# Optimization experiments

Hardware: AMD Instinct MI355X
Metric: run time of the kernel (lower is better)

The kernel has to match this reference:

```python
import jax, jax.numpy as jnp
import numpy as np

HEADS = 16
HEAD_DIM = 64
EMBED = HEADS * HEAD_DIM  # 1024
B, S = 2, 2048


def setup_inputs() -> dict:
    key = jax.random.key(0)
    ks = jax.random.split(key, 9)
    return {
        "value": jax.random.normal(ks[0], (B, S, EMBED), dtype=jnp.float32),
        "key": jax.random.normal(ks[1], (B, S, EMBED), dtype=jnp.float32),
        "query": jax.random.normal(ks[2], (B, S, EMBED), dtype=jnp.float32),
        "mask": jax.random.randint(ks[3], (B, 1, S, S), 0, 2, dtype=jnp.int32),
        "Wq": jax.random.normal(ks[4], (HEAD_DIM, HEAD_DIM), dtype=jnp.float32) * 0.02,
        "Wk": jax.random.normal(ks[5], (HEAD_DIM, HEAD_DIM), dtype=jnp.float32) * 0.02,
        "Wv": jax.random.normal(ks[6], (HEAD_DIM, HEAD_DIM), dtype=jnp.float32) * 0.02,
        "Wo": jax.random.normal(ks[7], (EMBED, EMBED), dtype=jnp.float32) * 0.02,
        "bo": jnp.zeros((EMBED,), dtype=jnp.float32),
    }


def reference(value, key, query, mask, Wq, Wk, Wv, Wo, bo):
    N, Lv = value.shape[0], value.shape[1]
    Lk, Lq = key.shape[1], query.shape[1]
    # Faithful to original: plain reshape (N, heads, len, head_dim), NOT transpose.
    v = value.reshape(N, HEADS, Lv, HEAD_DIM)
    k = key.reshape(N, HEADS, Lk, HEAD_DIM)
    q = query.reshape(N, HEADS, Lq, HEAD_DIM)
    # Per-head Linear (no bias): x @ W.T
    V = jnp.einsum('bhld,ed->bhle', v, Wv)
    K = jnp.einsum('bhld,ed->bhle', k, Wk)
    Q = jnp.einsum('bhld,ed->bhle', q, Wq)
    score = jnp.einsum('bhqd,bhkd->bhqk', Q, K)  # [B,H,Sq,Sk]
    score = jnp.where(mask == 0, jnp.float32(-1e20), score)
    # Faithful quirk: scale by sqrt(embed_size), not sqrt(head_dim)
    scale = jnp.float32(EMBED ** 0.5)
    attn = jax.nn.softmax(score / scale, axis=3)
    out = jnp.einsum('bhqk,bhkd->bhqd', attn, V).reshape(N, Lq, HEADS * HEAD_DIM)
    return out @ Wo.T + bo
```

## Files before the change

kernel.cpp:

```cpp
#include <hip/hip_runtime.h>
#include <hip/hip_bf16.h>
#include <cstdint>
#include <cstddef>

#define S_LEN 2048
#define N_HEADS 16
#define HD 64
#define EMB 1024
#define N_BATCH 2
#define N_BH (N_BATCH * N_HEADS)

typedef __attribute__((ext_vector_type(4))) float f32x4;
typedef __attribute__((ext_vector_type(8))) short short8;
typedef __attribute__((ext_vector_type(8))) _Float16 half8;
typedef __attribute__((ext_vector_type(2))) _Float16 half2v;

__device__ __forceinline__ f32x4 mfma16h(half8 a, half8 b, f32x4 c) {
    return __builtin_amdgcn_mfma_f32_16x16x32_f16(a, b, c, 0, 0, 0);
}

__device__ __forceinline__ unsigned pkh(float a, float b) {
    return __builtin_bit_cast(unsigned, __builtin_amdgcn_cvt_pkrtz(a, b));
}

#if __has_builtin(__builtin_amdgcn_exp2f)
__device__ __forceinline__ float fast_exp2(float x) { return __builtin_amdgcn_exp2f(x); }
#else
__device__ __forceinline__ float fast_exp2(float x) { return exp2f(x); }
#endif

__global__ __launch_bounds__(256) void prep_kernel(
    const float* __restrict__ q_in, const float* __restrict__ k_in,
    const float* __restrict__ v_in,
    const float* __restrict__ Wq, const float* __restrict__ Wk,
    const float* __restrict__ Wv, const float* __restrict__ Wo,
    const int* __restrict__ mask,
    short* __restrict__ Qb, short* __restrict__ Kb, short* __restrict__ Vt,
    short* __restrict__ Woh, unsigned long long* __restrict__ bits) {
    __shared__ short Al[64 * 72];
    __shared__ short Wl[64 * 72];
    __shared__ short Ol[64 * 72];
    int bx = blockIdx.x;
    int t = threadIdx.x;

    if (bx >= 3072) {
        if (bx < 11264) {
            int wid = ((bx - 3072) * 256 + t) >> 6;
            int lane = t & 63;
            const int* src = mask + (size_t)wid * 256 + lane;
            unsigned long long w0 = __ballot(src[0] != 0);
            unsigned long long w1 = __ballot(src[64] != 0);
            unsigned long long w2 = __ballot(src[128] != 0);
            unsigned long long w3 = __ballot(src[192] != 0);
            if (lane == 0) {
                unsigned long long* dst = bits + (size_t)wid * 4;
                dst[0] = w0; dst[1] = w1; dst[2] = w2; dst[3] = w3;
            }
        } else {
            int i = (bx - 11264) * 256 + t;
            f32x4 a = reinterpret_cast<const f32x4*>(Wo)[i * 2];
            f32x4 b = reinterpret_cast<const f32x4*>(Wo)[i * 2 + 1];
            uint4 u = { pkh(a.x, a.y), pkh(a.z, a.w), pkh(b.x, b.y), pkh(b.z, b.w) };
            reinterpret_cast<uint4*>(Woh)[i] = u;
        }
        return;
    }

    int rt = bx & 31;
    int bh = (bx >> 5) & 31;
    int tz = bx >> 10;
    const float* src = (tz == 0 ? q_in : tz == 1 ? k_in : v_in)
                       + (size_t)bh * S_LEN * HD + (size_t)rt * 64 * HD;
    const float* W = (tz == 0 ? Wq : tz == 1 ? Wk : Wv);

#pragma unroll
    for (int r = 0; r < 4; r++) {
        int f4 = t + 256 * r;
        int row = f4 >> 4;
        int c4 = (f4 & 15) * 4;
        f32x4 a = reinterpret_cast<const f32x4*>(src)[f4];
        uint2 ua = { pkh(a.x, a.y), pkh(a.z, a.w) };
        *reinterpret_cast<uint2*>(&Al[row * 72 + c4]) = ua;
        f32x4 w = reinterpret_cast<const f32x4*>(W)[f4];
        uint2 uw = { pkh(w.x, w.y), pkh(w.z, w.w) };
        *reinterpret_cast<uint2*>(&Wl[row * 72 + c4]) = uw;
    }
    __syncthreads();

    int wave = t >> 6, lane = t & 63, quad = lane >> 4, col = lane & 15;
    half8 a0 = *reinterpret_cast<const half8*>(&Al[(wave * 16 + col) * 72 + quad * 8]);
    half8 a1 = *reinterpret_cast<const half8*>(&Al[(wave * 16 + col) * 72 + 32 + quad * 8]);

    const float C1 = 0.04508422002777448f;
    float scl = (tz == 0) ? C1 : 1.0f;

    f32x4 acc[4];
#pragma unroll
    for (int jt = 0; jt < 4; jt++) {
        half8 b0 = *reinterpret_cast<const half8*>(&Wl[(jt * 16 + col) * 72 + quad * 8]);
        half8 b1 = *reinterpret_cast<const half8*>(&Wl[(jt * 16 + col) * 72 + 32 + quad * 8]);
        f32x4 c = {0.f, 0.f, 0.f, 0.f};
        c = mfma16h(a0, b0, c);
        c = mfma16h(a1, b1, c);
        acc[jt] = c;
    }
    __syncthreads();

    if (tz < 2) {
#pragma unroll
        for (int jt = 0; jt < 4; jt++)
#pragma unroll
            for (int i = 0; i < 4; i++)
                Ol[(wave * 16 + quad * 4 + i) * 72 + jt * 16 + col] =
                    __builtin_bit_cast(short, (_Float16)(acc[jt][i] * scl));
        __syncthreads();
        short* dst = (tz == 0 ? Qb : Kb) + (size_t)bh * S_LEN * HD + (size_t)rt * 64 * HD;
        int row = t >> 2, ck = (t & 3) * 16;
        short8 o0 = *reinterpret_cast<const short8*>(&Ol[row * 72 + ck]);
        short8 o1 = *reinterpret_cast<const short8*>(&Ol[row * 72 + ck + 8]);
        *reinterpret_cast<short8*>(&dst[row * 64 + ck]) = o0;
        *reinterpret_cast<short8*>(&dst[row * 64 + ck + 8]) = o1;
    } else {
#pragma unroll
        for (int jt = 0; jt < 4; jt++)
#pragma unroll
            for (int i = 0; i < 4; i++)
                Ol[(jt * 16 + col) * 72 + wave * 16 + quad * 4 + i] =
                    __builtin_bit_cast(short, (_Float16)acc[jt][i]);
        __syncthreads();
        short* dst = Vt + (size_t)bh * HD * S_LEN + rt * 64;
        int d = t >> 2, ck = (t & 3) * 16;
        short8 o0 = *reinterpret_cast<const short8*>(&Ol[d * 72 + ck]);
        short8 o1 = *reinterpret_cast<const short8*>(&Ol[d * 72 + ck + 8]);
        *reinterpret_cast<short8*>(&dst[(size_t)d * S_LEN + ck]) = o0;
        *reinterpret_cast<short8*>(&dst[(size_t)d * S_LEN + ck + 8]) = o1;
    }
}

__global__ __launch_bounds__(512, 4) void attn_kernel(
    const short* __restrict__ Qb, const short* __restrict__ Kb,
    const short* __restrict__ Vt, const unsigned long long* __restrict__ mbits,
    short* __restrict__ Xb) {
    int qt = blockIdx.x;
    int bh = blockIdx.y;
    int b = bh >> 4;
    int t = threadIdx.x, wave = t >> 6, lane = t & 63, quad = lane >> 4, col = lane & 15;

    __shared__ short Ks[64 * 64];
    __shared__ short Vs[64 * 64];
    __shared__ short Pl[8][16 * 72];
    short* Pw = &Pl[wave][0];

    const short* Qh = Qb + (size_t)bh * S_LEN * HD;
    const short* Kh = Kb + (size_t)bh * S_LEN * HD;
    const short* Vh = Vt + (size_t)bh * HD * S_LEN;
    int q0w = qt * 128 + wave * 16;
    int q = q0w + col;

    half8 qf0 = *reinterpret_cast<const half8*>(&Qh[(size_t)q * HD + quad * 8]);
    half8 qf1 = *reinterpret_cast<const half8*>(&Qh[(size_t)q * HD + 32 + quad * 8]);
    const unsigned long long* mrow = mbits + (size_t)(b * S_LEN + q) * 32;

    int r0 = t >> 3, cc = t & 7;
    int dst0 = r0 * 64 + ((cc ^ (r0 & 7)) * 8);
    const short* kg0 = Kh + r0 * HD + cc * 8;
    const short* vg0 = Vh + (size_t)r0 * S_LEN + cc * 8;

    short8 pk0 = *reinterpret_cast<const short8*>(kg0);
    short8 pv0 = *reinterpret_cast<const short8*>(vg0);
    *reinterpret_cast<short8*>(&Ks[dst0]) = pk0;
    *reinterpret_cast<short8*>(&Vs[dst0]) = pv0;
    __syncthreads();

    unsigned bs[4];
#pragma unroll
    for (int i = 0; i < 4; i++) bs[i] = 1u << (quad * 4 + i);
    half8 ones = { (_Float16)1.f, (_Float16)1.f, (_Float16)1.f, (_Float16)1.f,
                   (_Float16)1.f, (_Float16)1.f, (_Float16)1.f, (_Float16)1.f };

    int sw = quad ^ (col & 7);
    unsigned long long mw = mrow[0];

    f32x4 o[4];
    f32x4 l = {0.f, 0.f, 0.f, 0.f};
#pragma unroll
    for (int dt = 0; dt < 4; dt++) o[dt] = (f32x4){0.f, 0.f, 0.f, 0.f};

    for (int kt = 0; kt < 32; kt++) {
        unsigned long long mw_n;
        if (kt < 31) {
            pk0 = *reinterpret_cast<const short8*>(kg0 + (kt + 1) * 4096);
            pv0 = *reinterpret_cast<const short8*>(vg0 + (kt + 1) * 64);
            mw_n = mrow[kt + 1];
        }
        f32x4 s[4];
#pragma unroll
        for (int mt = 0; mt < 4; mt++) {
            const short* kbase = &Ks[(mt * 16 + col) * 64];
            half8 ka0 = *reinterpret_cast<const half8*>(&kbase[sw * 8]);
            half8 ka1 = *reinterpret_cast<const half8*>(&kbase[(sw ^ 4) * 8]);
            f32x4 c = {0.f, 0.f, 0.f, 0.f};
            c = mfma16h(ka0, qf0, c);
            c = mfma16h(ka1, qf1, c);
            s[mt] = c;
        }
#pragma unroll
        for (int mt = 0; mt < 4; mt++) {
            unsigned g = (unsigned)(mw >> (mt * 16));
            float p0 = fast_exp2((g & bs[0]) ? s[mt][0] : -200.0f);
            float p1 = fast_exp2((g & bs[1]) ? s[mt][1] : -200.0f);
            float p2 = fast_exp2((g & bs[2]) ? s[mt][2] : -200.0f);
            float p3 = fast_exp2((g & bs[3]) ? s[mt][3] : -200.0f);
            uint2 dw = { pkh(p0, p1), pkh(p2, p3) };
            *reinterpret_cast<uint2*>(&Pw[col * 72 + mt * 16 + quad * 4]) = dw;
        }
#pragma unroll
        for (int c = 0; c < 2; c++) {
            half8 pb = *reinterpret_cast<const half8*>(&Pw[col * 72 + c * 32 + quad * 8]);
            l = mfma16h(ones, pb, l);
#pragma unroll
            for (int dt = 0; dt < 4; dt++) {
                half8 va = *reinterpret_cast<const half8*>(
                    &Vs[(dt * 16 + col) * 64 + (((c * 4 + quad) ^ (col & 7)) * 8)]);
                o[dt] = mfma16h(va, pb, o[dt]);
            }
        }
        __syncthreads();
        if (kt < 31) {
            *reinterpret_cast<short8*>(&Ks[dst0]) = pk0;
            *reinterpret_cast<short8*>(&Vs[dst0]) = pv0;
            mw = mw_n;
            __syncthreads();
        }
    }

    float inv = 1.0f / l[0];
#pragma unroll
    for (int dt = 0; dt < 4; dt++) {
        uint2 dw = { pkh(o[dt][0] * inv, o[dt][1] * inv),
                     pkh(o[dt][2] * inv, o[dt][3] * inv) };
        *reinterpret_cast<uint2*>(&Pw[col * 72 + dt * 16 + quad * 4]) = dw;
    }
    int rr = lane >> 2, ck = (lane & 3) * 16;
    short8 x0 = *reinterpret_cast<const short8*>(&Pw[rr * 72 + ck]);
    short8 x1 = *reinterpret_cast<const short8*>(&Pw[rr * 72 + ck + 8]);
    short* Xrow = Xb + (size_t)bh * S_LEN * HD + (size_t)(q0w + rr) * HD;
    *reinterpret_cast<short8*>(&Xrow[ck]) = x0;
    *reinterpret_cast<short8*>(&Xrow[ck + 8]) = x1;
}

__global__ __launch_bounds__(256, 4) void final_kernel(
    const short* __restrict__ Xb, const short* __restrict__ Woh,
    const float* __restrict__ bo, float* __restrict__ out) {
    int nb = blockIdx.x;
    int mb = blockIdx.y;
    int t = threadIdx.x, wave = t >> 6, lane = t & 63, quad = lane >> 4, col = lane & 15;
    __shared__ short Xs[64 * 64];
    __shared__ short Ws[64 * 64];
    __shared__ float Olds[64 * 68];

    int m0 = mb * 64, n0 = nb * 64;
    int r0 = t >> 3, r1 = (t + 256) >> 3, cc = t & 7;
    int dst0 = r0 * 64 + ((cc ^ (r0 & 7)) * 8);
    int dst1 = r1 * 64 + ((cc ^ (r1 & 7)) * 8);
    const short* xg0 = Xb + (size_t)(m0 + r0) * EMB + cc * 8;
    const short* xg1 = Xb + (size_t)(m0 + r1) * EMB + cc * 8;
    const short* wg0 = Woh + (size_t)(n0 + r0) * EMB + cc * 8;
    const short* wg1 = Woh + (size_t)(n0 + r1) * EMB + cc * 8;

    short8 px0 = *reinterpret_cast<const short8*>(xg0);
    short8 px1 = *reinterpret_cast<const short8*>(xg1);
    short8 pw0 = *reinterpret_cast<const short8*>(wg0);
    short8 pw1 = *reinterpret_cast<const short8*>(wg1);
    *reinterpret_cast<short8*>(&Xs[dst0]) = px0;
    *reinterpret_cast<short8*>(&Xs[dst1]) = px1;
    *reinterpret_cast<short8*>(&Ws[dst0]) = pw0;
    *reinterpret_cast<short8*>(&Ws[dst1]) = pw1;
    __syncthreads();

    int sw = quad ^ (col & 7);
    f32x4 acc[4];
#pragma unroll
    for (int jt = 0; jt < 4; jt++) acc[jt] = (f32x4){0.f, 0.f, 0.f, 0.f};

    for (int s = 0; s < 16; s++) {
        if (s < 15) {
            px0 = *reinterpret_cast<const short8*>(xg0 + (s + 1) * 64);
            px1 = *reinterpret_cast<const short8*>(xg1 + (s + 1) * 64);
            pw0 = *reinterpret_cast<const short8*>(wg0 + (s + 1) * 64);
            pw1 = *reinterpret_cast<const short8*>(wg1 + (s + 1) * 64);
        }
        const short* arow = &Xs[(wave * 16 + col) * 64];
        half8 a0 = *reinterpret_cast<const half8*>(&arow[sw * 8]);
        half8 a1 = *reinterpret_cast<const half8*>(&arow[(sw ^ 4) * 8]);
#pragma unroll
        for (int jt = 0; jt < 4; jt++) {
            const short* brow = &Ws[(jt * 16 + col) * 64];
            half8 b0 = *reinterpret_cast<const half8*>(&brow[sw * 8]);
            half8 b1 = *reinterpret_cast<const half8*>(&brow[(sw ^ 4) * 8]);
            acc[jt] = mfma16h(a0, b0, acc[jt]);
            acc[jt] = mfma16h(a1, b1, acc[jt]);
        }
        __syncthreads();
        if (s < 15) {
            *reinterpret_cast<short8*>(&Xs[dst0]) = px0;
            *reinterpret_cast<short8*>(&Xs[dst1]) = px1;
            *reinterpret_cast<short8*>(&Ws[dst0]) = pw0;
            *reinterpret_cast<short8*>(&Ws[dst1]) = pw1;
            __syncthreads();
        }
    }

#pragma unroll
    for (int jt = 0; jt < 4; jt++)
#pragma unroll
        for (int i = 0; i < 4; i++)
            Olds[(wave * 16 + quad * 4 + i) * 68 + jt * 16 + col] = acc[jt][i];
    __syncthreads();
    int row = t >> 2, ck = (t & 3) * 16;
#pragma unroll
    for (int u = 0; u < 4; u++) {
        f32x4 v = *reinterpret_cast<const f32x4*>(&Olds[row * 68 + ck + u * 4]);
        f32x4 bb = *reinterpret_cast<const f32x4*>(&bo[n0 + ck + u * 4]);
        v.x += bb.x; v.y += bb.y; v.z += bb.z; v.w += bb.w;
        *reinterpret_cast<f32x4*>(&out[(size_t)(m0 + row) * EMB + n0 + ck + u * 4]) = v;
    }
}

extern "C" void kernel_launch(void* const* d_in, const int* in_sizes, int n_in,
                              void* d_out, int out_size, void* d_ws, size_t ws_size,
                              hipStream_t stream) {
    const float* value = (const float*)d_in[0];
    const float* key_  = (const float*)d_in[1];
    const float* query = (const float*)d_in[2];
    const int*   mask  = (const int*)d_in[3];
    const float* Wq = (const float*)d_in[4];
    const float* Wk = (const float*)d_in[5];
    const float* Wv = (const float*)d_in[6];
    const float* Wo = (const float*)d_in[7];
    const float* bo = (const float*)d_in[8];
    float* out = (float*)d_out;

    char* ws = (char*)d_ws;
    short* Qb  = (short*)(ws);
    short* Kb  = (short*)(ws + (size_t)8  * 1048576);
    short* Vt  = (short*)(ws + (size_t)16 * 1048576);
    short* Xb  = (short*)(ws + (size_t)24 * 1048576);
    short* Woh = (short*)(ws + (size_t)32 * 1048576);
    unsigned long long* mbits =
        (unsigned long long*)(ws + (size_t)34 * 1048576);

    prep_kernel<<<dim3(3072 + 8192 + 512), dim3(256), 0, stream>>>(
        query, key_, value, Wq, Wk, Wv, Wo, mask, Qb, Kb, Vt, Woh, mbits);
    attn_kernel<<<dim3(S_LEN / 128, N_BH), dim3(512), 0, stream>>>(Qb, Kb, Vt, mbits, Xb);
    final_kernel<<<dim3(EMB / 64, (N_BATCH * S_LEN) / 64), dim3(256), 0, stream>>>(
        Xb, Woh, bo, out);
}
```

Before: 204.7 us.

## Switch attention to 32x32 MFMA with split-K waves, double buffering, and retiled output GEMM

Measured after the change: 212.7 us. 3.9% more time.

```diff
diff --git a/kernel.cpp b/kernel.cpp
--- a/kernel.cpp
+++ b/kernel.cpp
@@ -11,12 +11,15 @@
 #define N_BH (N_BATCH * N_HEADS)
 
 typedef __attribute__((ext_vector_type(4))) float f32x4;
+typedef __attribute__((ext_vector_type(16))) float f32x16;
 typedef __attribute__((ext_vector_type(8))) short short8;
 typedef __attribute__((ext_vector_type(8))) _Float16 half8;
-typedef __attribute__((ext_vector_type(2))) _Float16 half2v;
 
 __device__ __forceinline__ f32x4 mfma16h(half8 a, half8 b, f32x4 c) {
     return __builtin_amdgcn_mfma_f32_16x16x32_f16(a, b, c, 0, 0, 0);
+}
+__device__ __forceinline__ f32x16 mfma32h(half8 a, half8 b, f32x16 c) {
+    return __builtin_amdgcn_mfma_f32_32x32x16_f16(a, b, c, 0, 0, 0);
 }
 
 __device__ __forceinline__ unsigned pkh(float a, float b) {
@@ -44,20 +47,21 @@
     int t = threadIdx.x;
 
     if (bx >= 3072) {
-        if (bx < 11264) {
-            int wid = ((bx - 3072) * 256 + t) >> 6;
+        if (bx < 5120) {
+            int gw = (bx - 3072) * 4 + (t >> 6);
             int lane = t & 63;
-            const int* src = mask + (size_t)wid * 256 + lane;
-            unsigned long long w0 = __ballot(src[0] != 0);
-            unsigned long long w1 = __ballot(src[64] != 0);
-            unsigned long long w2 = __ballot(src[128] != 0);
-            unsigned long long w3 = __ballot(src[192] != 0);
-            if (lane == 0) {
-                unsigned long long* dst = bits + (size_t)wid * 4;
-                dst[0] = w0; dst[1] = w1; dst[2] = w2; dst[3] = w3;
+            const int* src = mask + (size_t)gw * 1024 + lane;
+            int row = gw >> 1;
+            int bb = row >> 11, qq = row & 2047;
+            int wbase = (gw & 1) * 16;
+#pragma unroll
+            for (int r = 0; r < 16; r++) {
+                unsigned long long w = __ballot(src[r * 64] != 0);
+                if (lane == 0)
+                    bits[((size_t)(bb * 32 + wbase + r) << 11) + qq] = w;
             }
         } else {
-            int i = (bx - 11264) * 256 + t;
+            int i = (bx - 5120) * 256 + t;
             f32x4 a = reinterpret_cast<const f32x4*>(Wo)[i * 2];
             f32x4 b = reinterpret_cast<const f32x4*>(Wo)[i * 2 + 1];
             uint4 u = { pkh(a.x, a.y), pkh(a.z, a.w), pkh(b.x, b.y), pkh(b.z, b.w) };
@@ -144,186 +148,198 @@
     int qt = blockIdx.x;
     int bh = blockIdx.y;
     int b = bh >> 4;
-    int t = threadIdx.x, wave = t >> 6, lane = t & 63, quad = lane >> 4, col = lane & 15;
-
-    __shared__ short Ks[64 * 64];
-    __shared__ short Vs[64 * 64];
-    __shared__ short Pl[8][16 * 72];
-    short* Pw = &Pl[wave][0];
+    int t = threadIdx.x, wave = t >> 6, lane = t & 63;
+    int g = wave & 3, h = wave >> 2;
+    int l5 = lane >> 5, l31 = lane & 31;
+
+    __shared__ short smem[26880];
+    short* Pg = smem + 16384 + wave * 1280;
 
     const short* Qh = Qb + (size_t)bh * S_LEN * HD;
     const short* Kh = Kb + (size_t)bh * S_LEN * HD;
     const short* Vh = Vt + (size_t)bh * HD * S_LEN;
-    int q0w = qt * 128 + wave * 16;
-    int q = q0w + col;
-
-    half8 qf0 = *reinterpret_cast<const half8*>(&Qh[(size_t)q * HD + quad * 8]);
-    half8 qf1 = *reinterpret_cast<const half8*>(&Qh[(size_t)q * HD + 32 + quad * 8]);
-    const unsigned long long* mrow = mbits + (size_t)(b * S_LEN + q) * 32;
+    int qbase = qt * 128 + g * 32;
+    int q = qbase + l31;
+
+    half8 qf[4];
+#pragma unroll
+    for (int kc = 0; kc < 4; kc++)
+        qf[kc] = *reinterpret_cast<const half8*>(&Qh[(size_t)q * HD + kc * 16 + l5 * 8]);
+
+    const unsigned long long* mcol = mbits + ((size_t)(b * 32) << 11);
+    unsigned long long mwq = mcol[q];
 
     int r0 = t >> 3, cc = t & 7;
-    int dst0 = r0 * 64 + ((cc ^ (r0 & 7)) * 8);
+    int dstoff = r0 * 64 + ((cc ^ (r0 & 7)) * 8);
     const short* kg0 = Kh + r0 * HD + cc * 8;
     const short* vg0 = Vh + (size_t)r0 * S_LEN + cc * 8;
 
-    short8 pk0 = *reinterpret_cast<const short8*>(kg0);
-    short8 pv0 = *reinterpret_cast<const short8*>(vg0);
-    *reinterpret_cast<short8*>(&Ks[dst0]) = pk0;
-    *reinterpret_cast<short8*>(&Vs[dst0]) = pv0;
-    __syncthreads();
-
-    unsigned bs[4];
-#pragma unroll
-    for (int i = 0; i < 4; i++) bs[i] = 1u << (quad * 4 + i);
-    half8 ones = { (_Float16)1.f, (_Float16)1.f, (_Float16)1.f, (_Float16)1.f,
-                   (_Float16)1.f, (_Float16)1.f, (_Float16)1.f, (_Float16)1.f };
-
-    int sw = quad ^ (col & 7);
-    unsigned long long mw = mrow[0];
-
-    f32x4 o[4];
-    f32x4 l = {0.f, 0.f, 0.f, 0.f};
-#pragma unroll
-    for (int dt = 0; dt < 4; dt++) o[dt] = (f32x4){0.f, 0.f, 0.f, 0.f};
+    short8 pk = *reinterpret_cast<const short8*>(kg0);
+    short8 pv = *reinterpret_cast<const short8*>(vg0);
+    *reinterpret_cast<short8*>(&smem[dstoff]) = pk;
+    *reinterpret_cast<short8*>(&smem[4096 + dstoff]) = pv;
+    __syncthreads();
+
+    f32x16 o0, o1;
+#pragma unroll
+    for (int r = 0; r < 16; r++) { o0[r] = 0.f; o1[r] = 0.f; }
+    float l_acc = 0.f;
+    int krow = h * 32 + l31;
 
     for (int kt = 0; kt < 32; kt++) {
-        unsigned long long mw_n;
+        unsigned long long mwq_n;
         if (kt < 31) {
-            pk0 = *reinterpret_cast<const short8*>(kg0 + (kt + 1) * 4096);
-            pv0 = *reinterpret_cast<const short8*>(vg0 + (kt + 1) * 64);
-            mw_n = mrow[kt + 1];
-        }
-        f32x4 s[4];
-#pragma unroll
-        for (int mt = 0; mt < 4; mt++) {
-            const short* kbase = &Ks[(mt * 16 + col) * 64];
-            half8 ka0 = *reinterpret_cast<const half8*>(&kbase[sw * 8]);
-            half8 ka1 = *reinterpret_cast<const half8*>(&kbase[(sw ^ 4) * 8]);
-            f32x4 c = {0.f, 0.f, 0.f, 0.f};
-            c = mfma16h(ka0, qf0, c);
-            c = mfma16h(ka1, qf1, c);
-            s[mt] = c;
-        }
-#pragma unroll
-        for (int mt = 0; mt < 4; mt++) {
-            unsigned g = (unsigned)(mw >> (mt * 16));
-            float p0 = fast_exp2((g & bs[0]) ? s[mt][0] : -200.0f);
-            float p1 = fast_exp2((g & bs[1]) ? s[mt][1] : -200.0f);
-            float p2 = fast_exp2((g & bs[2]) ? s[mt][2] : -200.0f);
-            float p3 = fast_exp2((g & bs[3]) ? s[mt][3] : -200.0f);
-            uint2 dw = { pkh(p0, p1), pkh(p2, p3) };
-            *reinterpret_cast<uint2*>(&Pw[col * 72 + mt * 16 + quad * 4]) = dw;
+            pk = *reinterpret_cast<const short8*>(kg0 + (kt + 1) * 4096);
+            pv = *reinterpret_cast<const short8*>(vg0 + (kt + 1) * 64);
+            mwq_n = mcol[((size_t)(kt + 1) << 11) + q];
+        }
+        const short* Kbs = smem + (kt & 1) * 8192;
+        const short* Vbs = Kbs + 4096;
+
+        f32x16 s;
+#pragma unroll
+        for (int r = 0; r < 16; r++) s[r] = 0.f;
+#pragma unroll
+        for (int kc = 0; kc < 4; kc++) {
+            half8 ka = *reinterpret_cast<const half8*>(
+                &Kbs[krow * 64 + (((kc * 2 + l5) ^ (krow & 7)) * 8)]);
+            s = mfma32h(ka, qf[kc], s);
+        }
+        unsigned gs = (unsigned)(mwq >> (h * 32)) >> (4 * l5);
+        float p[16];
+#pragma unroll
+        for (int r = 0; r < 16; r++) {
+            int bitc = (r & 3) + 8 * (r >> 2);
+            p[r] = fast_exp2(((gs >> bitc) & 1u) ? s[r] : -200.0f);
+            l_acc += p[r];
+        }
+#pragma unroll
+        for (int u = 0; u < 4; u++) {
+            uint2 dw = { pkh(p[4 * u], p[4 * u + 1]), pkh(p[4 * u + 2], p[4 * u + 3]) };
+            *reinterpret_cast<uint2*>(&Pg[l31 * 40 + 4 * l5 + 8 * u]) = dw;
         }
 #pragma unroll
         for (int c = 0; c < 2; c++) {
-            half8 pb = *reinterpret_cast<const half8*>(&Pw[col * 72 + c * 32 + quad * 8]);
-            l = mfma16h(ones, pb, l);
-#pragma unroll
-            for (int dt = 0; dt < 4; dt++) {
+            half8 pb = *reinterpret_cast<const half8*>(&Pg[l31 * 40 + c * 16 + l5 * 8]);
+            {
+                int vrow = l31;
                 half8 va = *reinterpret_cast<const half8*>(
-                    &Vs[(dt * 16 + col) * 64 + (((c * 4 + quad) ^ (col & 7)) * 8)]);
-                o[dt] = mfma16h(va, pb, o[dt]);
+                    &Vbs[vrow * 64 + (((h * 4 + c * 2 + l5) ^ (vrow & 7)) * 8)]);
+                o0 = mfma32h(va, pb, o0);
             }
+            {
+                int vrow = 32 + l31;
+                half8 va = *reinterpret_cast<const half8*>(
+                    &Vbs[vrow * 64 + (((h * 4 + c * 2 + l5) ^ (vrow & 7)) * 8)]);
+                o1 = mfma32h(va, pb, o1);
+            }
+        }
+        if (kt < 31) {
+            short* nb = smem + ((kt + 1) & 1) * 8192;
+            *reinterpret_cast<short8*>(&nb[dstoff]) = pk;
+            *reinterpret_cast<short8*>(&nb[4096 + dstoff]) = pv;
+            mwq = mwq_n;
         }
         __syncthreads();
-        if (kt < 31) {
-            *reinterpret_cast<short8*>(&Ks[dst0]) = pk0;
-            *reinterpret_cast<short8*>(&Vs[dst0]) = pv0;
-            mw = mw_n;
-            __syncthreads();
-        }
-    }
-
-    float inv = 1.0f / l[0];
-#pragma unroll
-    for (int dt = 0; dt < 4; dt++) {
-        uint2 dw = { pkh(o[dt][0] * inv, o[dt][1] * inv),
-                     pkh(o[dt][2] * inv, o[dt][3] * inv) };
-        *reinterpret_cast<uint2*>(&Pw[col * 72 + dt * 16 + quad * 4]) = dw;
-    }
-    int rr = lane >> 2, ck = (lane & 3) * 16;
-    short8 x0 = *reinterpret_cast<const short8*>(&Pw[rr * 72 + ck]);
-    short8 x1 = *reinterpret_cast<const short8*>(&Pw[rr * 72 + ck + 8]);
-    short* Xrow = Xb + (size_t)bh * S_LEN * HD + (size_t)(q0w + rr) * HD;
-    *reinterpret_cast<short8*>(&Xrow[ck]) = x0;
-    *reinterpret_cast<short8*>(&Xrow[ck + 8]) = x1;
-}
-
-__global__ __launch_bounds__(256, 4) void final_kernel(
+    }
+
+    l_acc += __shfl_xor(l_acc, 32);
+    float* obuf = (float*)smem;
+    float* lbuf = (float*)(smem + 26624);
+    if (h == 1) {
+#pragma unroll
+        for (int r = 0; r < 16; r++) {
+            obuf[(g * 32 + r) * 64 + lane] = o0[r];
+            obuf[(g * 32 + 16 + r) * 64 + lane] = o1[r];
+        }
+        if (lane < 32) lbuf[g * 32 + lane] = l_acc;
+    }
+    __syncthreads();
+    if (h == 0) {
+        float inv = 1.0f / (l_acc + lbuf[g * 32 + l31]);
+#pragma unroll
+        for (int r = 0; r < 16; r++) {
+            o0[r] = (o0[r] + obuf[(g * 32 + r) * 64 + lane]) * inv;
+            o1[r] = (o1[r] + obuf[(g * 32 + 16 + r) * 64 + lane]) * inv;
+        }
+        short* Xrow = Xb + (size_t)bh * S_LEN * HD + (size_t)q * HD;
+#pragma unroll
+        for (int u = 0; u < 4; u++) {
+            uint2 w0 = { pkh(o0[4 * u], o0[4 * u + 1]), pkh(o0[4 * u + 2], o0[4 * u + 3]) };
+            *reinterpret_cast<uint2*>(&Xrow[4 * l5 + 8 * u]) = w0;
+            uint2 w1 = { pkh(o1[4 * u], o1[4 * u + 1]), pkh(o1[4 * u + 2], o1[4 * u + 3]) };
+            *reinterpret_cast<uint2*>(&Xrow[32 + 4 * l5 + 8 * u]) = w1;
+        }
+    }
+}
+
+__global__ __launch_bounds__(512, 4) void final_kernel(
     const short* __restrict__ Xb, const short* __restrict__ Woh,
     const float* __restrict__ bo, float* __restrict__ out) {
     int nb = blockIdx.x;
     int mb = blockIdx.y;
     int t = threadIdx.x, wave = t >> 6, lane = t & 63, quad = lane >> 4, col = lane & 15;
-    __shared__ short Xs[64 * 64];
-    __shared__ short Ws[64 * 64];
-    __shared__ float Olds[64 * 68];
-
-    int m0 = mb * 64, n0 = nb * 64;
-    int r0 = t >> 3, r1 = (t + 256) >> 3, cc = t & 7;
-    int dst0 = r0 * 64 + ((cc ^ (r0 & 7)) * 8);
-    int dst1 = r1 * 64 + ((cc ^ (r1 & 7)) * 8);
+    __shared__ short smem[24576];
+
+    int m0 = mb * 128, n0 = nb * 64;
+    int r0 = t >> 3, r1 = r0 + 64, cc = t & 7;
+    int dx0 = r0 * 64 + ((cc ^ (r0 & 7)) * 8);
+    int dx1 = r1 * 64 + ((cc ^ (r1 & 7)) * 8);
     const short* xg0 = Xb + (size_t)(m0 + r0) * EMB + cc * 8;
     const short* xg1 = Xb + (size_t)(m0 + r1) * EMB + cc * 8;
     const short* wg0 = Woh + (size_t)(n0 + r0) * EMB + cc * 8;
-    const short* wg1 = Woh + (size_t)(n0 + r1) * EMB + cc * 8;
 
     short8 px0 = *reinterpret_cast<const short8*>(xg0);
     short8 px1 = *reinterpret_cast<const short8*>(xg1);
     short8 pw0 = *reinterpret_cast<const short8*>(wg0);
-    short8 pw1 = *reinterpret_cast<const short8*>(wg1);
-    *reinterpret_cast<short8*>(&Xs[dst0]) = px0;
-    *reinterpret_cast<short8*>(&Xs[dst1]) = px1;
-    *reinterpret_cast<short8*>(&Ws[dst0]) = pw0;
-    *reinterpret_cast<short8*>(&Ws[dst1]) = pw1;
-    __syncthreads();
-
-    int sw = quad ^ (col & 7);
+    *reinterpret_cast<short8*>(&smem[dx0]) = px0;
+    *reinterpret_cast<short8*>(&smem[dx1]) = px1;
+    *reinterpret_cast<short8*>(&smem[16384 + dx0]) = pw0;
+    __syncthreads();
+
     f32x4 acc[4];
 #pragma unroll
-    for (int jt = 0; jt < 4; jt++) acc[jt] = (f32x4){0.f, 0.f, 0.f, 0.f};
+    for (int nf = 0; nf < 4; nf++) acc[nf] = (f32x4){0.f, 0.f, 0.f, 0.f};
+    int arow = wave * 16 + col;
 
     for (int s = 0; s < 16; s++) {
         if (s < 15) {
             px0 = *reinterpret_cast<const short8*>(xg0 + (s + 1) * 64);
             px1 = *reinterpret_cast<const short8*>(xg1 + (s + 1) * 64);
             pw0 = *reinterpret_cast<const short8*>(wg0 + (s + 1) * 64);
-            pw1 = *reinterpret_cast<const short8*>(wg1 + (s + 1) * 64);
-        }
-        const short* arow = &Xs[(wave * 16 + col) * 64];
-        half8 a0 = *reinterpret_cast<const half8*>(&arow[sw * 8]);
-        half8 a1 = *reinterpret_cast<const half8*>(&arow[(sw ^ 4) * 8]);
-#pragma unroll
-        for (int jt = 0; jt < 4; jt++) {
-            const short* brow = &Ws[(jt * 16 + col) * 64];
-            half8 b0 = *reinterpret_cast<const half8*>(&brow[sw * 8]);
-            half8 b1 = *reinterpret_cast<const half8*>(&brow[(sw ^ 4) * 8]);
-            acc[jt] = mfma16h(a0, b0, acc[jt]);
-            acc[jt] = mfma16h(a1, b1, acc[jt]);
+        }
+        const short* Xs = smem + (s & 1) * 8192;
+        const short* Ws = smem + 16384 + (s & 1) * 4096;
+#pragma unroll
+        for (int k2 = 0; k2 < 2; k2++) {
+            half8 a = *reinterpret_cast<const half8*>(
+                &Xs[arow * 64 + (((k2 * 4 + quad) ^ (arow & 7)) * 8)]);
+#pragma unroll
+            for (int nf = 0; nf < 4; nf++) {
+                int brow = nf * 16 + col;
+                half8 bf = *reinterpret_cast<const half8*>(
+                    &Ws[brow * 64 + (((k2 * 4 + quad) ^ (brow & 7)) * 8)]);
+                acc[nf] = mfma16h(a, bf, acc[nf]);
+            }
+        }
+        if (s < 15) {
+            short* Xn = smem + ((s + 1) & 1) * 8192;
+            short* Wn = smem + 16384 + ((s + 1) & 1) * 4096;
+            *reinterpret_cast<short8*>(&Xn[dx0]) = px0;
+            *reinterpret_cast<short8*>(&Xn[dx1]) = px1;
+            *reinterpret_cast<short8*>(&Wn[dx0]) = pw0;
         }
         __syncthreads();
-        if (s < 15) {
-            *reinterpret_cast<short8*>(&Xs[dst0]) = px0;
-            *reinterpret_cast<short8*>(&Xs[dst1]) = px1;
-            *reinterpret_cast<short8*>(&Ws[dst0]) = pw0;
-            *reinterpret_cast<short8*>(&Ws[dst1]) = pw1;
-            __syncthreads();
-        }
-    }
-
-#pragma unroll
-    for (int jt = 0; jt < 4; jt++)
+    }
+
+#pragma unroll
+    for (int nf = 0; nf < 4; nf++) {
+        int n = n0 + nf * 16 + col;
+        float bb = bo[n];
+        int rowb = m0 + wave * 16 + quad * 4;
 #pragma unroll
         for (int i = 0; i < 4; i++)
-            Olds[(wave * 16 + quad * 4 + i) * 68 + jt * 16 + col] = acc[jt][i];
-    __syncthreads();
-    int row = t >> 2, ck = (t & 3) * 16;
-#pragma unroll
-    for (int u = 0; u < 4; u++) {
-        f32x4 v = *reinterpret_cast<const f32x4*>(&Olds[row * 68 + ck + u * 4]);
-        f32x4 bb = *reinterpret_cast<const f32x4*>(&bo[n0 + ck + u * 4]);
-        v.x += bb.x; v.y += bb.y; v.z += bb.z; v.w += bb.w;
-        *reinterpret_cast<f32x4*>(&out[(size_t)(m0 + row) * EMB + n0 + ck + u * 4]) = v;
+            out[(size_t)(rowb + i) * EMB + n] = acc[nf][i] + bb;
     }
 }
 
@@ -350,9 +366,9 @@
     unsigned long long* mbits =
         (unsigned long long*)(ws + (size_t)34 * 1048576);
 
-    prep_kernel<<<dim3(3072 + 8192 + 512), dim3(256), 0, stream>>>(
+    prep_kernel<<<dim3(3072 + 2048 + 512), dim3(256), 0, stream>>>(
         query, key_, value, Wq, Wk, Wv, Wo, mask, Qb, Kb, Vt, Woh, mbits);
     attn_kernel<<<dim3(S_LEN / 128, N_BH), dim3(512), 0, stream>>>(Qb, Kb, Vt, mbits, Xb);
-    final_kernel<<<dim3(EMB / 64, (N_BATCH * S_LEN) / 64), dim3(256), 0, stream>>>(
+    final_kernel<<<dim3(EMB / 64, (N_BATCH * S_LEN) / 128), dim3(512), 0, stream>>>(
         Xb, Woh, bo, out);
 }
```
